# Kernel optimization log

Measured on AMD Instinct MI355X. Metric: run time of the kernel, lower is better.

Reference implementation:

```python
import jax, jax.numpy as jnp
import numpy as np

H = 12  # num_heads
LN_EPS = 1e-5


def setup_inputs() -> dict:
    key = jax.random.key(0)
    ks = jax.random.split(key, 9)
    B, N, C = 16, 785, 768
    hd = C // H
    s = lambda k, shp, fan: jax.random.normal(k, shp, jnp.float32) * (1.0 / np.sqrt(fan))
    return {
        "x": jax.random.normal(ks[0], (B, N, C), jnp.float32),
        "qkv_w": s(ks[1], (C, 3 * C), C),          # Linear(dim, 3*dim), no bias
        "proj_w": s(ks[2], (C, C), C),
        "proj_b": jnp.zeros((C,), jnp.float32),
        "htp_w": s(ks[3], (hd, C), hd),            # ht_proj: Linear(hd, dim)
        "htp_b": jnp.zeros((C,), jnp.float32),
        "ln_g": jnp.ones((hd,), jnp.float32),      # ht_norm LayerNorm(hd)
        "ln_b": jnp.zeros((hd,), jnp.float32),
        "pos": jax.random.normal(ks[4], (1, H, C), jnp.float32) * 0.02,
    }


def reference(x, qkv_w, proj_w, proj_b, htp_w, htp_b, ln_g, ln_b, pos):
    B, N, C = x.shape
    hd = C // H
    scale = hd ** -0.5

    # head-token construction: per-head mean pool over tokens -> (B, H, hd)
    xh = x.reshape(B, N, H, hd).mean(axis=1)
    ht = (xh @ htp_w + htp_b).reshape(B, H, H, hd)        # ht_proj then split per head
    mu = ht.mean(axis=-1, keepdims=True)
    var = ht.var(axis=-1, keepdims=True)
    ht = (ht - mu) * jax.lax.rsqrt(var + LN_EPS) * ln_g + ln_b
    ht = jax.nn.gelu(ht, approximate=False).reshape(B, H, C) + pos  # + head pos embed

    xa = jnp.concatenate([x, ht], axis=1)                 # (B, T, C), T = N + H
    T = N + H

    qkv = (xa @ qkv_w).reshape(B, T, 3, H, hd)
    q, k, v = (jnp.moveaxis(qkv, 2, 0)[i].transpose(0, 2, 1, 3) for i in range(3))  # (B,H,T,hd)
    attn = jax.nn.softmax(jnp.einsum("bhqd,bhkd->bhqk", q, k) * scale, axis=-1)
    out = jnp.einsum("bhqk,bhkd->bhqd", attn, v).transpose(0, 2, 1, 3).reshape(B, T, C)
    out = out @ proj_w + proj_b

    cls = out[:, :1] + out[:, N:].mean(axis=1, keepdims=True)  # cls += mean of head tokens
    return jnp.concatenate([cls, out[:, 1:N]], axis=1)         # (B, N, C)
```

## Files before the change

### kernel.cpp

```cpp
#include <hip/hip_runtime.h>
#include <hip/hip_bf16.h>
#include <math.h>

#define Bsz 16
#define Ntok 785
#define Cdim 768
#define Hn 12
#define HD 64
#define Ttok 797
#define Kdim 768
#define K3C 2304
#define LN_EPS 1e-5f
#define Mrows (Bsz * Ttok)
#define NQS 3
#define NPARTS 5

typedef _Float16 f16;
typedef __attribute__((ext_vector_type(8))) _Float16 half8;
typedef __attribute__((ext_vector_type(4))) _Float16 half4v;
typedef __attribute__((ext_vector_type(8))) unsigned short ushort8;
typedef __attribute__((ext_vector_type(4))) float f32x4;

__device__ inline float wave_sum(float v) {
    #pragma unroll
    for (int off = 32; off; off >>= 1) v += __shfl_xor(v, off, 64);
    return v;
}

#define SW(row) (((((row) & 7) ^ (((row) >> 3) & 7))) << 3)

__global__ void prep_x(const float* __restrict__ x, f16* __restrict__ xa,
                       float* __restrict__ partial) {
    int b = blockIdx.x, ch = blockIdx.y, t = threadIdx.x;
    int n0 = ch * 50, n1 = min(Ntok, n0 + 50);
    float s0 = 0.f, s1 = 0.f, s2 = 0.f;
    for (int n = n0; n < n1; ++n) {
        const float* row = x + ((size_t)b * Ntok + n) * Cdim;
        f16* orow = xa + ((size_t)b * Ttok + n) * Cdim;
        float v0 = row[t], v1 = row[t + 256], v2 = row[t + 512];
        s0 += v0; s1 += v1; s2 += v2;
        orow[t] = (f16)v0; orow[t + 256] = (f16)v1; orow[t + 512] = (f16)v2;
    }
    float* p = partial + ((size_t)b * 16 + ch) * Cdim;
    p[t] = s0; p[t + 256] = s1; p[t + 512] = s2;
}

__global__ void headtok_kernel(const float* __restrict__ partial, const float* __restrict__ htp_w,
                               const float* __restrict__ htp_b, const float* __restrict__ ln_g,
                               const float* __restrict__ ln_b, const float* __restrict__ pos,
                               f16* __restrict__ xa) {
    int blk = blockIdx.x;
    int b  = blk / (Hn * Hn);
    int rem = blk % (Hn * Hn);
    int h  = rem / Hn;
    int h2 = rem % Hn;
    int lane = threadIdx.x;
    int c = h2 * HD + lane;

    float sx = 0.f;
    #pragma unroll
    for (int ch = 0; ch < 16; ++ch)
        sx += partial[((size_t)b * 16 + ch) * Cdim + h * HD + lane];
    float xv = sx * (1.0f / (float)Ntok);

    float acc = htp_b[c];
    #pragma unroll 8
    for (int d = 0; d < HD; ++d) acc += __shfl(xv, d, 64) * htp_w[(size_t)d * Cdim + c];

    float mu = wave_sum(acc) * (1.0f / 64.0f);
    float diff = acc - mu;
    float var = wave_sum(diff * diff) * (1.0f / 64.0f);
    float y = diff * rsqrtf(var + LN_EPS) * ln_g[lane] + ln_b[lane];
    float g = 0.5f * y * (1.0f + erff(y * 0.70710678118654752f));
    float v = g + pos[(size_t)h * Cdim + c];
    xa[((size_t)b * Ttok + Ntok + h) * Cdim + c] = (f16)v;
}

__global__ void convert_both(const float* __restrict__ Wq, f16* __restrict__ WTq,
                             const float* __restrict__ Wp, f16* __restrict__ WTp) {
    __shared__ float tile[32][33];
    int bx = blockIdx.x;
    const float* W; f16* WT; int N, nt;
    if (bx < K3C / 32) { W = Wq; WT = WTq; N = K3C; nt = bx * 32; }
    else               { W = Wp; WT = WTp; N = Cdim; nt = (bx - K3C / 32) * 32; }
    int kt = blockIdx.y * 32;
    int tx = threadIdx.x & 31, ty = threadIdx.x >> 5;
    #pragma unroll
    for (int r = 0; r < 32; r += 8)
        tile[ty + r][tx] = W[(size_t)(kt + ty + r) * N + nt + tx];
    __syncthreads();
    #pragma unroll
    for (int r = 0; r < 32; r += 8) {
        int n = nt + ty + r, k = kt + tx;
        WT[(size_t)n * Kdim + k] = (f16)tile[tx][ty + r];
    }
}

__global__ __launch_bounds__(256, 4)
void mfma_gemm(const f16* __restrict__ A, const f16* __restrict__ W,
               const float* __restrict__ bias, int M, int Nn, int mode, int nNb,
               float* __restrict__ outF, float* __restrict__ sbuf,
               f16* __restrict__ outH) {
    __shared__ __align__(16) f16 smem[2][2][4096];
    const int idx = blockIdx.x;
    const int xcd = idx & 7;
    const int sidx = idx >> 3;
    const int mloc = sidx % 13;
    const int nb = sidx / 13;
    const int cnt = (xcd < 4) ? 13 : 12;
    if (mloc >= cnt) return;
    const int mb = (xcd < 4 ? xcd * 13 : 52 + (xcd - 4) * 12) + mloc;
    const int mBase = mb * 128, nBase = nb * 128;

    const int tid = threadIdx.x;
    const int w = tid >> 6, lane = tid & 63;
    const int lr = lane & 15, lg = lane >> 4;
    const int wr = w >> 1, wc = w & 1;

    const f16* src = (w < 2) ? A : W;
    const int arr = w >> 1;
    const int rowOff = (w & 1) * 64;
    const int rowBase = (w < 2) ? mBase : nBase;
    const int rowMax  = (w < 2) ? (M - 1) : (Nn - 1);
    const int cg = (lane & 3) ^ ((lane >> 3) & 3);
    const int sl8 = (lg ^ ((lr >> 1) & 3)) * 8;

    f32x4 acc[4][4];
    #pragma unroll
    for (int mi = 0; mi < 4; ++mi)
        #pragma unroll
        for (int ni = 0; ni < 4; ++ni) {
            acc[mi][ni][0] = 0.f; acc[mi][ni][1] = 0.f;
            acc[mi][ni][2] = 0.f; acc[mi][ni][3] = 0.f;
        }

    auto stage = [&](int buf, int k0) {
        #pragma unroll
        for (int i = 0; i < 4; ++i) {
            int r16 = rowOff + i * 16;
            int grow = min(rowBase + r16 + (lane >> 2), rowMax);
            const f16* g = src + (size_t)grow * Kdim + k0 + cg * 8;
            f16* l = &smem[buf][arr][r16 * 32];
            __builtin_amdgcn_global_load_lds(
                (const __attribute__((address_space(1))) void*)g,
                (__attribute__((address_space(3))) void*)l, 16, 0, 0);
        }
    };

    const int NT = Kdim / 32;
    stage(0, 0);
    stage(1, 32);
    asm volatile("s_waitcnt vmcnt(4)" ::: "memory");
    __builtin_amdgcn_sched_barrier(0);
    __builtin_amdgcn_s_barrier();
    __builtin_amdgcn_sched_barrier(0);

    for (int t = 0; t < NT; ++t) {
        const f16* AS = &smem[t & 1][0][0];
        const f16* WS = &smem[t & 1][1][0];
        half8 a[4], b[4];
        #pragma unroll
        for (int mi = 0; mi < 4; ++mi)
            a[mi] = *reinterpret_cast<const half8*>(&AS[(wr * 64 + mi * 16 + lr) * 32 + sl8]);
        #pragma unroll
        for (int ni = 0; ni < 4; ++ni)
            b[ni] = *reinterpret_cast<const half8*>(&WS[(wc * 64 + ni * 16 + lr) * 32 + sl8]);
        #pragma unroll
        for (int mi = 0; mi < 4; ++mi)
            #pragma unroll
            for (int ni = 0; ni < 4; ++ni)
                acc[mi][ni] = __builtin_amdgcn_mfma_f32_16x16x32_f16(a[mi], b[ni], acc[mi][ni], 0, 0, 0);

        if (t + 1 < NT) {
            asm volatile("s_waitcnt vmcnt(0) lgkmcnt(0)" ::: "memory");
            __builtin_amdgcn_sched_barrier(0);
            __builtin_amdgcn_s_barrier();
            __builtin_amdgcn_sched_barrier(0);
            if (t + 2 < NT) stage(t & 1, (t + 2) * 32);
        }
    }

    if (mode == 0) {
        #pragma unroll
        for (int ni = 0; ni < 4; ++ni) {
            int gn = nBase + wc * 64 + ni * 16 + lr;
            float bv = bias ? bias[gn] : 0.f;
            #pragma unroll
            for (int mi = 0; mi < 4; ++mi)
                #pragma unroll
                for (int r = 0; r < 4; ++r) {
                    int gm = mBase + wr * 64 + mi * 16 + lg * 4 + r;
                    if (gm < M) {
                        int bb = gm / Ttok, tt = gm - bb * Ttok;
                        float v = acc[mi][ni][r] + bv;
                        if (tt >= 1 && tt < Ntok)
                            outF[((size_t)bb * Ntok + tt) * Nn + gn] = v;
                        else
                            sbuf[((size_t)bb * 13 + (tt == 0 ? 0 : tt - Ntok + 1)) * Nn + gn] = v;
                    }
                }
        }
    } else {
        __syncthreads();
        f16* Ew = &smem[0][0][0] + (size_t)w * 4096;
        #pragma unroll
        for (int mi = 0; mi < 4; ++mi)
            #pragma unroll
            for (int ni = 0; ni < 4; ++ni)
                #pragma unroll
                for (int r = 0; r < 4; ++r) {
                    int er = mi * 16 + lg * 4 + r;
                    int ec = ni * 16 + lr;
                    int chunk = ec >> 3;
                    Ew[er * 64 + ((chunk ^ (er & 7)) << 3) + (ec & 7)] = (f16)acc[mi][ni][r];
                }
        __syncthreads();
        int scol = nBase + wc * 64;
        int s = scol / Cdim;
        int hc = scol - s * Cdim;
        int h = hc >> 6;
        #pragma unroll
        for (int c8 = 0; c8 < 8; ++c8) {
            int er = (lane >> 3) + c8 * 8;
            int chunk = lane & 7;
            half8 v = *reinterpret_cast<const half8*>(&Ew[er * 64 + ((chunk ^ (er & 7)) << 3)]);
            int gm = mBase + wr * 64 + er;
            if (gm < M) {
                int bb = gm / Ttok, tt = gm - bb * Ttok;
                f16* dst = outH + (((size_t)(s * Bsz + bb) * Hn + h) * Ttok + tt) * HD + chunk * 8;
                *reinterpret_cast<half8*>(dst) = v;
            }
        }
    }
}

__global__ __launch_bounds__(256, 2)
void flash_attn_kernel(const f16* __restrict__ Qb, const f16* __restrict__ Kb,
                       const f16* __restrict__ Vb, f16* __restrict__ ao) {
    __shared__ __align__(16) unsigned short KS[2][64 * 64];
    __shared__ __align__(16) unsigned short VS[2][64 * 64];

    int bh   = blockIdx.x % (Bsz * Hn);
    int part = blockIdx.x / (Bsz * Hn);
    int st   = 3 * part - (part == 4 ? 1 : 0);
    int q0   = st * 64;
    int smax = (part < 3) ? 3 : 2;
    int tid = threadIdx.x;
    int w = tid >> 6, lane = tid & 63;
    int lr = lane & 15, lg = lane >> 4;
    size_t base = (size_t)bh * Ttok * HD;

    half8 qf[NQS][2];
    #pragma unroll
    for (int s = 0; s < NQS; ++s) {
        int qrow = q0 + s * 64 + w * 16 + lr;
        int crow = min(qrow, Ttok - 1);
        #pragma unroll
        for (int kf = 0; kf < 2; ++kf)
            qf[s][kf] = *reinterpret_cast<const half8*>(Qb + base + (size_t)crow * HD + kf * 32 + lg * 8);
    }

    f32x4 O[NQS][4];
    float lsum[NQS];
    #pragma unroll
    for (int s = 0; s < NQS; ++s) {
        lsum[s] = 0.f;
        #pragma unroll
        for (int nt = 0; nt < 4; ++nt) { O[s][nt][0]=0.f; O[s][nt][1]=0.f; O[s][nt][2]=0.f; O[s][nt][3]=0.f; }
    }

    const unsigned short* Kg = (const unsigned short*)(Kb + base);
    const unsigned short* Vg = (const unsigned short*)(Vb + base);

    int pr = tid >> 3;
    int g  = tid & 7;
    int k0 = 2 * pr, k1 = k0 + 1;

    ushort8 kv0, kv1, vv0, vv1;
    auto load_tile = [&](int kt) {
        int gk0 = kt * 64 + k0;
        if (kt < 12) {
            kv0 = *reinterpret_cast<const ushort8*>(&Kg[(size_t)gk0 * HD + g * 8]);
            vv0 = *reinterpret_cast<const ushort8*>(&Vg[(size_t)gk0 * HD + g * 8]);
            kv1 = *reinterpret_cast<const ushort8*>(&Kg[(size_t)(gk0 + 1) * HD + g * 8]);
            vv1 = *reinterpret_cast<const ushort8*>(&Vg[(size_t)(gk0 + 1) * HD + g * 8]);
        } else {
            ushort8 z;
            #pragma unroll
            for (int jj = 0; jj < 8; ++jj) z[jj] = 0;
            kv0 = z; vv0 = z; kv1 = z; vv1 = z;
            if (gk0 < Ttok) {
                kv0 = *reinterpret_cast<const ushort8*>(&Kg[(size_t)gk0 * HD + g * 8]);
                vv0 = *reinterpret_cast<const ushort8*>(&Vg[(size_t)gk0 * HD + g * 8]);
            }
            if (gk0 + 1 < Ttok) {
                kv1 = *reinterpret_cast<const ushort8*>(&Kg[(size_t)(gk0 + 1) * HD + g * 8]);
                vv1 = *reinterpret_cast<const ushort8*>(&Vg[(size_t)(gk0 + 1) * HD + g * 8]);
            }
        }
    };
    auto write_tile = [&](int buf) {
        *reinterpret_cast<ushort8*>(&KS[buf][(k0 * 64 + g * 8) ^ SW(k0)]) = kv0;
        *reinterpret_cast<ushort8*>(&KS[buf][(k1 * 64 + g * 8) ^ SW(k1)]) = kv1;
        unsigned* VTd = reinterpret_cast<unsigned*>(&VS[buf][0]);
        #pragma unroll
        for (int jj = 0; jj < 8; ++jj) {
            int dim = g * 8 + jj;
            unsigned w2 = (unsigned)vv0[jj] | ((unsigned)vv1[jj] << 16);
            VTd[dim * 32 + (pr ^ ((((dim & 7) ^ ((dim >> 3) & 7))) << 2))] = w2;
        }
    };

    load_tile(0);
    write_tile(0);
    load_tile(1);
    asm volatile("s_waitcnt lgkmcnt(0)" ::: "memory");
    __builtin_amdgcn_sched_barrier(0);
    __builtin_amdgcn_s_barrier();
    __builtin_amdgcn_sched_barrier(0);

    for (int kt = 0; kt < 13; ++kt) {
        bool tail = (kt == 12);
        int cur = kt & 1;
        const unsigned short* KSc = &KS[cur][0];
        const unsigned short* VSc = &VS[cur][0];

        int kbase = kt * 64;
        #pragma unroll
        for (int s = 0; s < NQS; ++s) {
            if (s < smax) {
                half4v pa[4];
                float ls = 0.f;
                #pragma unroll
                for (int ntk = 0; ntk < 4; ++ntk) {
                    f32x4 sc; sc[0]=0.f; sc[1]=0.f; sc[2]=0.f; sc[3]=0.f;
                    #pragma unroll
                    for (int kf = 0; kf < 2; ++kf) {
                        int key = ntk * 16 + lr;
                        int d0 = kf * 32 + lg * 8;
                        half8 k8 = *reinterpret_cast<const half8*>(
                            reinterpret_cast<const f16*>(&KSc[(key * 64 + d0) ^ SW(key)]));
                        sc = __builtin_amdgcn_mfma_f32_16x16x32_f16(k8, qf[s][kf], sc, 0, 0, 0);
                    }
                    float p[4];
                    if (!tail) {
                        #pragma unroll
                        for (int r = 0; r < 4; ++r) {
                            p[r] = __expf(sc[r] * 0.125f - 6.0f);
                            ls += p[r];
                        }
                    } else {
                        int kb2 = kbase + ntk * 16 + lg * 4;
                        #pragma unroll
                        for (int r = 0; r < 4; ++r) {
                            bool valid = (kb2 + r) < Ttok;
                            p[r] = valid ? __expf(sc[r] * 0.125f - 6.0f) : 0.f;
                            ls += p[r];
                        }
                    }
                    auto lo = __builtin_amdgcn_cvt_pkrtz(p[0], p[1]);
                    auto hi = __builtin_amdgcn_cvt_pkrtz(p[2], p[3]);
                    pa[ntk][0] = (f16)lo[0]; pa[ntk][1] = (f16)lo[1];
                    pa[ntk][2] = (f16)hi[0]; pa[ntk][3] = (f16)hi[1];
                }
                lsum[s] += ls;
                #pragma unroll
                for (int ntd = 0; ntd < 4; ++ntd) {
                    int dim = ntd * 16 + lr;
                    #pragma unroll
                    for (int ntk = 0; ntk < 4; ++ntk) {
                        half4v v4 = *reinterpret_cast<const half4v*>(
                            reinterpret_cast<const f16*>(&VSc[(dim * 64 + ntk * 16 + lg * 4) ^ SW(dim)]));
                        O[s][ntd] = __builtin_amdgcn_mfma_f32_16x16x16f16(pa[ntk], v4, O[s][ntd], 0, 0, 0);
                    }
                }
            }
        }

        if (kt + 1 < 13) {
            write_tile((kt + 1) & 1);
            if (kt + 2 < 13) load_tile(kt + 2);
            asm volatile("s_waitcnt lgkmcnt(0)" ::: "memory");
            __builtin_amdgcn_sched_barrier(0);
            __builtin_amdgcn_s_barrier();
            __builtin_amdgcn_sched_barrier(0);
        }
    }

    __syncthreads();
    int b = bh / Hn, h = bh % Hn;
    f16* Ew = reinterpret_cast<f16*>(&KS[0][(size_t)w * 1024]);
    #pragma unroll
    for (int s = 0; s < NQS; ++s) {
        if (s < smax) {
            float l = lsum[s];
            l += __shfl_xor(l, 16, 64);
            l += __shfl_xor(l, 32, 64);
            float inv[4];
            #pragma unroll
            for (int r = 0; r < 4; ++r)
                inv[r] = 1.0f / __shfl(l, lg * 4 + r, 64);
            #pragma unroll
            for (int nt = 0; nt < 4; ++nt)
                #pragma unroll
                for (int r = 0; r < 4; ++r)
                    Ew[(lg * 4 + r) * 64 + nt * 16 + lr] = (f16)(O[s][nt][r] * inv[r]);
            int row = lane >> 2, seg = lane & 3;
            half8 v0 = *reinterpret_cast<const half8*>(&Ew[row * 64 + seg * 16]);
            half8 v1 = *reinterpret_cast<const half8*>(&Ew[row * 64 + seg * 16 + 8]);
            int qrow = q0 + s * 64 + w * 16 + row;
            if (qrow < Ttok) {
                f16* dst = ao + ((size_t)b * Ttok + qrow) * Cdim + h * HD + seg * 16;
                *reinterpret_cast<half8*>(dst) = v0;
                *reinterpret_cast<half8*>(dst + 8) = v1;
            }
        }
    }
}

__global__ void cls2_kernel(const float* __restrict__ sbuf, float* __restrict__ out) {
    int b = blockIdx.x, t = threadIdx.x;
    #pragma unroll
    for (int i = 0; i < 3; ++i) {
        int c = t + i * 256;
        float s = sbuf[((size_t)b * 13) * Cdim + c];
        float hs = 0.f;
        #pragma unroll
        for (int h = 0; h < Hn; ++h)
            hs += sbuf[((size_t)b * 13 + 1 + h) * Cdim + c];
        out[((size_t)b * Ntok) * Cdim + c] = s + hs * (1.0f / (float)Hn);
    }
}

extern "C" void kernel_launch(void* const* d_in, const int* in_sizes, int n_in,
                              void* d_out, int out_size, void* d_ws, size_t ws_size,
                              hipStream_t stream) {
    const float* x      = (const float*)d_in[0];
    const float* qkv_w  = (const float*)d_in[1];
    const float* proj_w = (const float*)d_in[2];
    const float* proj_b = (const float*)d_in[3];
    const float* htp_w  = (const float*)d_in[4];
    const float* htp_b  = (const float*)d_in[5];
    const float* ln_g   = (const float*)d_in[6];
    const float* ln_b   = (const float*)d_in[7];
    const float* pos    = (const float*)d_in[8];
    float* out = (float*)d_out;

    const size_t MC = (size_t)Mrows * Cdim;
    const size_t WQ = (size_t)K3C * Kdim;
    const size_t WP = (size_t)Cdim * Kdim;

    f16* qkv   = (f16*)d_ws;
    f16* xa    = qkv + 3 * MC;
    f16* wq    = xa + MC;
    f16* wp    = wq + WQ;
    float* partial = (float*)(wp + WP);
    float* sbuf    = partial + (size_t)Bsz * 16 * Cdim;

    prep_x<<<dim3(Bsz, 16), 256, 0, stream>>>(x, xa, partial);
    headtok_kernel<<<Bsz * Hn * Hn, 64, 0, stream>>>(partial, htp_w, htp_b, ln_g, ln_b, pos, xa);
    convert_both<<<dim3(96, Kdim / 32), 256, 0, stream>>>(qkv_w, wq, proj_w, wp);

    mfma_gemm<<<8 * 13 * 18, 256, 0, stream>>>(
        xa, wq, nullptr, Mrows, K3C, 1, 18, nullptr, nullptr, qkv);

    flash_attn_kernel<<<Bsz * Hn * NPARTS, 256, 0, stream>>>(
        qkv, qkv + MC, qkv + 2 * MC, xa);

    mfma_gemm<<<8 * 13 * 6, 256, 0, stream>>>(
        xa, wp, proj_b, Mrows, Cdim, 0, 6, out, sbuf, nullptr);

    cls2_kernel<<<Bsz, 256, 0, stream>>>(sbuf, out);
}
```

Baseline: 185.7 us.

## Widen GEMM tile to 128x256 with each wave covering full M

New measurement: 186.7 us. Within noise of the previous version (+0.5%).

```diff
diff --git a/kernel.cpp b/kernel.cpp
--- a/kernel.cpp
+++ b/kernel.cpp
@@ -96,12 +96,12 @@
     }
 }
 
-__global__ __launch_bounds__(256, 4)
+__global__ __launch_bounds__(256, 2)
 void mfma_gemm(const f16* __restrict__ A, const f16* __restrict__ W,
                const float* __restrict__ bias, int M, int Nn, int mode, int nNb,
                float* __restrict__ outF, float* __restrict__ sbuf,
                f16* __restrict__ outH) {
-    __shared__ __align__(16) f16 smem[2][2][4096];
+    __shared__ __align__(16) f16 smem[2][12288];
     const int idx = blockIdx.x;
     const int xcd = idx & 7;
     const int sidx = idx >> 3;
@@ -110,24 +110,24 @@
     const int cnt = (xcd < 4) ? 13 : 12;
     if (mloc >= cnt) return;
     const int mb = (xcd < 4 ? xcd * 13 : 52 + (xcd - 4) * 12) + mloc;
-    const int mBase = mb * 128, nBase = nb * 128;
+    const int mBase = mb * 128, nBase = nb * 256;
 
     const int tid = threadIdx.x;
     const int w = tid >> 6, lane = tid & 63;
     const int lr = lane & 15, lg = lane >> 4;
-    const int wr = w >> 1, wc = w & 1;
 
     const f16* src = (w < 2) ? A : W;
-    const int arr = w >> 1;
-    const int rowOff = (w & 1) * 64;
+    const int rowOff = (w < 2) ? (w * 64) : ((w - 2) * 128);
+    const int nInstr = (w < 2) ? 4 : 8;
+    const int ldsOff = (w < 2) ? 0 : 4096;
     const int rowBase = (w < 2) ? mBase : nBase;
     const int rowMax  = (w < 2) ? (M - 1) : (Nn - 1);
     const int cg = (lane & 3) ^ ((lane >> 3) & 3);
     const int sl8 = (lg ^ ((lr >> 1) & 3)) * 8;
 
-    f32x4 acc[4][4];
-    #pragma unroll
-    for (int mi = 0; mi < 4; ++mi)
+    f32x4 acc[8][4];
+    #pragma unroll
+    for (int mi = 0; mi < 8; ++mi)
         #pragma unroll
         for (int ni = 0; ni < 4; ++ni) {
             acc[mi][ni][0] = 0.f; acc[mi][ni][1] = 0.f;
@@ -135,12 +135,11 @@
         }
 
     auto stage = [&](int buf, int k0) {
-        #pragma unroll
-        for (int i = 0; i < 4; ++i) {
+        for (int i = 0; i < nInstr; ++i) {
             int r16 = rowOff + i * 16;
             int grow = min(rowBase + r16 + (lane >> 2), rowMax);
             const f16* g = src + (size_t)grow * Kdim + k0 + cg * 8;
-            f16* l = &smem[buf][arr][r16 * 32];
+            f16* l = &smem[buf][ldsOff + r16 * 32];
             __builtin_amdgcn_global_load_lds(
                 (const __attribute__((address_space(1))) void*)g,
                 (__attribute__((address_space(3))) void*)l, 16, 0, 0);
@@ -150,23 +149,23 @@
     const int NT = Kdim / 32;
     stage(0, 0);
     stage(1, 32);
-    asm volatile("s_waitcnt vmcnt(4)" ::: "memory");
+    asm volatile("s_waitcnt vmcnt(0)" ::: "memory");
     __builtin_amdgcn_sched_barrier(0);
     __builtin_amdgcn_s_barrier();
     __builtin_amdgcn_sched_barrier(0);
 
     for (int t = 0; t < NT; ++t) {
-        const f16* AS = &smem[t & 1][0][0];
-        const f16* WS = &smem[t & 1][1][0];
-        half8 a[4], b[4];
-        #pragma unroll
-        for (int mi = 0; mi < 4; ++mi)
-            a[mi] = *reinterpret_cast<const half8*>(&AS[(wr * 64 + mi * 16 + lr) * 32 + sl8]);
+        const f16* AS = &smem[t & 1][0];
+        const f16* BS = &smem[t & 1][4096];
+        half8 a[8], b[4];
+        #pragma unroll
+        for (int mi = 0; mi < 8; ++mi)
+            a[mi] = *reinterpret_cast<const half8*>(&AS[(mi * 16 + lr) * 32 + sl8]);
         #pragma unroll
         for (int ni = 0; ni < 4; ++ni)
-            b[ni] = *reinterpret_cast<const half8*>(&WS[(wc * 64 + ni * 16 + lr) * 32 + sl8]);
-        #pragma unroll
-        for (int mi = 0; mi < 4; ++mi)
+            b[ni] = *reinterpret_cast<const half8*>(&BS[(w * 64 + ni * 16 + lr) * 32 + sl8]);
+        #pragma unroll
+        for (int mi = 0; mi < 8; ++mi)
             #pragma unroll
             for (int ni = 0; ni < 4; ++ni)
                 acc[mi][ni] = __builtin_amdgcn_mfma_f32_16x16x32_f16(a[mi], b[ni], acc[mi][ni], 0, 0, 0);
@@ -183,13 +182,13 @@
     if (mode == 0) {
         #pragma unroll
         for (int ni = 0; ni < 4; ++ni) {
-            int gn = nBase + wc * 64 + ni * 16 + lr;
+            int gn = nBase + w * 64 + ni * 16 + lr;
             float bv = bias ? bias[gn] : 0.f;
             #pragma unroll
-            for (int mi = 0; mi < 4; ++mi)
+            for (int mi = 0; mi < 8; ++mi)
                 #pragma unroll
                 for (int r = 0; r < 4; ++r) {
-                    int gm = mBase + wr * 64 + mi * 16 + lg * 4 + r;
+                    int gm = mBase + mi * 16 + lg * 4 + r;
                     if (gm < M) {
                         int bb = gm / Ttok, tt = gm - bb * Ttok;
                         float v = acc[mi][ni][r] + bv;
@@ -201,34 +200,37 @@
                 }
         }
     } else {
-        __syncthreads();
-        f16* Ew = &smem[0][0][0] + (size_t)w * 4096;
-        #pragma unroll
-        for (int mi = 0; mi < 4; ++mi)
-            #pragma unroll
-            for (int ni = 0; ni < 4; ++ni)
-                #pragma unroll
-                for (int r = 0; r < 4; ++r) {
-                    int er = mi * 16 + lg * 4 + r;
-                    int ec = ni * 16 + lr;
-                    int chunk = ec >> 3;
-                    Ew[er * 64 + ((chunk ^ (er & 7)) << 3) + (ec & 7)] = (f16)acc[mi][ni][r];
-                }
-        __syncthreads();
-        int scol = nBase + wc * 64;
+        f16* Ew = &smem[0][0] + (size_t)w * 4096;
+        int scol = nBase + w * 64;
         int s = scol / Cdim;
         int hc = scol - s * Cdim;
         int h = hc >> 6;
         #pragma unroll
-        for (int c8 = 0; c8 < 8; ++c8) {
-            int er = (lane >> 3) + c8 * 8;
-            int chunk = lane & 7;
-            half8 v = *reinterpret_cast<const half8*>(&Ew[er * 64 + ((chunk ^ (er & 7)) << 3)]);
-            int gm = mBase + wr * 64 + er;
-            if (gm < M) {
-                int bb = gm / Ttok, tt = gm - bb * Ttok;
-                f16* dst = outH + (((size_t)(s * Bsz + bb) * Hn + h) * Ttok + tt) * HD + chunk * 8;
-                *reinterpret_cast<half8*>(dst) = v;
+        for (int half = 0; half < 2; ++half) {
+            __syncthreads();
+            #pragma unroll
+            for (int mi = 0; mi < 4; ++mi)
+                #pragma unroll
+                for (int ni = 0; ni < 4; ++ni)
+                    #pragma unroll
+                    for (int r = 0; r < 4; ++r) {
+                        int er = mi * 16 + lg * 4 + r;
+                        int ec = ni * 16 + lr;
+                        int chunk = ec >> 3;
+                        Ew[er * 64 + ((chunk ^ (er & 7)) << 3) + (ec & 7)] = (f16)acc[half * 4 + mi][ni][r];
+                    }
+            __syncthreads();
+            #pragma unroll
+            for (int c8 = 0; c8 < 8; ++c8) {
+                int er = (lane >> 3) + c8 * 8;
+                int chunk = lane & 7;
+                half8 v = *reinterpret_cast<const half8*>(&Ew[er * 64 + ((chunk ^ (er & 7)) << 3)]);
+                int gm = mBase + half * 64 + er;
+                if (gm < M) {
+                    int bb = gm / Ttok, tt = gm - bb * Ttok;
+                    f16* dst = outH + (((size_t)(s * Bsz + bb) * Hn + h) * Ttok + tt) * HD + chunk * 8;
+                    *reinterpret_cast<half8*>(dst) = v;
+                }
             }
         }
     }
@@ -461,14 +463,14 @@
     headtok_kernel<<<Bsz * Hn * Hn, 64, 0, stream>>>(partial, htp_w, htp_b, ln_g, ln_b, pos, xa);
     convert_both<<<dim3(96, Kdim / 32), 256, 0, stream>>>(qkv_w, wq, proj_w, wp);
 
-    mfma_gemm<<<8 * 13 * 18, 256, 0, stream>>>(
-        xa, wq, nullptr, Mrows, K3C, 1, 18, nullptr, nullptr, qkv);
+    mfma_gemm<<<8 * 13 * 9, 256, 0, stream>>>(
+        xa, wq, nullptr, Mrows, K3C, 1, 9, nullptr, nullptr, qkv);
 
     flash_attn_kernel<<<Bsz * Hn * NPARTS, 256, 0, stream>>>(
         qkv, qkv + MC, qkv + 2 * MC, xa);
 
-    mfma_gemm<<<8 * 13 * 6, 256, 0, stream>>>(
-        xa, wp, proj_b, Mrows, Cdim, 0, 6, out, sbuf, nullptr);
+    mfma_gemm<<<8 * 13 * 3, 256, 0, stream>>>(
+        xa, wp, proj_b, Mrows, Cdim, 0, 3, out, sbuf, nullptr);
 
     cls2_kernel<<<Bsz, 256, 0, stream>>>(sbuf, out);
 }
```
